# Kernel optimization log

Measured on AMD Instinct MI355X. Metric: run time of the kernel, lower is better.

Reference implementation:

```python
import jax, jax.numpy as jnp
import numpy as np

K = 16          # neighbors per point
POINTNUM = 2048 # opt.pointnum
B, N = 8, 2048


def _knn_concat(x, k):
    """x: [B,N,C] -> [B,N,k,2C] = concat(center, k-nearest neighbor feats)."""
    sq = jnp.sum(x * x, axis=-1)                                   # [B,N]
    d2 = sq[:, :, None] + sq[:, None, :] - 2.0 * jnp.einsum('bnc,bmc->bnm', x, x)
    _, idx = jax.lax.top_k(-d2, k)                                 # [B,N,k]
    nbr = jax.vmap(lambda xb, ib: xb[ib])(x, idx)                  # [B,N,k,C]
    ctr = jnp.broadcast_to(x[:, :, None, :], nbr.shape)
    return jnp.concatenate([ctr, nbr], axis=-1)


def _lin(x, w, b):
    return x @ w + b


lrelu = jax.nn.leaky_relu  # default negative_slope=0.01 matches nn.LeakyReLU()


def setup_inputs() -> dict:
    key = jax.random.key(0)
    ks = jax.random.split(key, 20)

    def w(k_, fi, fo):
        return jax.random.normal(k_, (fi, fo), jnp.float32) / np.sqrt(fi)

    inp = {
        'x': jax.random.normal(ks[0], (B, N, 3), jnp.float32),
        'h1w1': w(ks[1], 6, 16),   'h1b1': jnp.zeros((16,), jnp.float32),
        'h1w2': w(ks[2], 16, 64),  'h1b2': jnp.zeros((64,), jnp.float32),
        'h1w3': w(ks[3], 64, 32),  'h1b3': jnp.zeros((32,), jnp.float32),
        'h2w1': w(ks[4], 64, 256), 'h2b1': jnp.zeros((256,), jnp.float32),
        'h2w2': w(ks[5], 256, 128),'h2b2': jnp.zeros((128,), jnp.float32),
        'h3w1': w(ks[6], 256, 128),'h3b1': jnp.zeros((128,), jnp.float32),
        'fc1w': w(ks[7], 128, 128),'fc1b': jnp.zeros((128,), jnp.float32),
        'fc2w': w(ks[8], 128, 128),'fc2b': jnp.zeros((128,), jnp.float32),
        'fc3w': w(ks[9], 128, POINTNUM * 3), 'fc3b': jnp.zeros((POINTNUM * 3,), jnp.float32),
    }
    return inp


def reference(x, h1w1, h1b1, h1w2, h1b2, h1w3, h1b3,
              h2w1, h2b1, h2w2, h2b2, h3w1, h3b1,
              fc1w, fc1b, fc2w, fc2b, fc3w, fc3b):
    # block 1: knn-concat [B,N,K,6] -> MLP(6,16,64,32) -> sum over K
    x1 = _knn_concat(x, K)
    h = lrelu(_lin(x1, h1w1, h1b1))
    h = lrelu(_lin(h, h1w2, h1b2))
    h = lrelu(_lin(h, h1w3, h1b3))
    x2 = jnp.sum(h, axis=2)                    # [B,N,32]
    # block 2: [B,N,K,64] -> MLP(64,256,128) -> sum over K
    x2 = _knn_concat(x2, K)
    h = lrelu(_lin(x2, h2w1, h2b1))
    h = lrelu(_lin(h, h2w2, h2b2))
    x3 = jnp.sum(h, axis=2)                    # [B,N,128]
    # block 3: [B,N,K,256] -> MLP(256,128) -> sum over K
    x3 = _knn_concat(x3, K)
    h = lrelu(_lin(x3, h3w1, h3b1))
    x4 = jnp.sum(h, axis=2)                    # [B,N,128]
    # global max pool over points
    x5 = jnp.max(x4, axis=1)                   # [B,128]
    x6 = lrelu(_lin(x5, fc1w, fc1b))
    x7 = lrelu(_lin(x6, fc2w, fc2b))
    x8 = _lin(x7, fc3w, fc3b)                  # [B, POINTNUM*3]
    return x8.reshape(x8.shape[0], POINTNUM, 3)
```

## Files before the change

kernel.cpp:

```cpp
#include <hip/hip_runtime.h>

#define KNB 16
#define BSZ 8
#define NPT 2048

typedef __attribute__((ext_vector_type(8))) short bf16x8;
typedef __attribute__((ext_vector_type(4))) float f32x4;

__device__ __forceinline__ float lrelu(float x) { return x >= 0.f ? x : 0.01f * x; }

__device__ __forceinline__ unsigned short bf16rne(float f) {
    union { float f; unsigned int u; } v; v.f = f;
    return (unsigned short)((v.u + 0x7FFFu + ((v.u >> 16) & 1u)) >> 16);
}

__device__ __forceinline__ float packkey(float d, int idx) {
    union { float f; unsigned int u; } v; v.f = d;
    v.u = (v.u & 0xFFFFF800u) | (unsigned int)idx;
    return v.f;
}

__device__ __forceinline__ void ceA(float& a, float& b) {
    const float lo = fminf(a, b), hi = fmaxf(a, b);
    a = lo; b = hi;
}

__device__ __forceinline__ void bsort16(float* c) {
#pragma unroll
    for (int k = 2; k <= 16; k <<= 1) {
#pragma unroll
        for (int j = k >> 1; j > 0; j >>= 1) {
#pragma unroll
            for (int i = 0; i < 16; ++i) {
                const int l = i ^ j;
                if (l > i) {
                    if ((i & k) == 0) ceA(c[i], c[l]);
                    else              ceA(c[l], c[i]);
                }
            }
        }
    }
}

__device__ __forceinline__ void merge16(float* L, const float* C) {
#pragma unroll
    for (int i = 0; i < 16; ++i) L[i] = fminf(L[i], C[15 - i]);
#pragma unroll
    for (int j = 8; j > 0; j >>= 1) {
#pragma unroll
        for (int i = 0; i < 16; ++i) {
            const int l = i ^ j;
            if (l > i) ceA(L[i], L[l]);
        }
    }
}

__device__ __forceinline__ void st16(float* dst, const float* L) {
#pragma unroll
    for (int c = 0; c < 4; ++c)
        *(f32x4*)(dst + c * 4) = (f32x4){L[c * 4], L[c * 4 + 1], L[c * 4 + 2], L[c * 4 + 3]};
}

__device__ __forceinline__ void ld16(float* L, const float* src) {
#pragma unroll
    for (int c = 0; c < 4; ++c) {
        const f32x4 v = *(const f32x4*)(src + c * 4);
        L[c * 4] = v[0]; L[c * 4 + 1] = v[1]; L[c * 4 + 2] = v[2]; L[c * 4 + 3] = v[3];
    }
}

__device__ __forceinline__ void xwave_merge_out(float (*sS)[20], int w, int lane,
                                                float* L, float* outp) {
    st16(sS[w * 64 + lane], L);
    __syncthreads();
    if ((w & 1) == 0) {
        float C[16];
        ld16(C, sS[(w + 1) * 64 + lane]);
        merge16(L, C);
        if (w == 2) st16(sS[2 * 64 + lane], L);
    }
    __syncthreads();
    if (w == 0) {
        float C[16];
        ld16(C, sS[2 * 64 + lane]);
        merge16(L, C);
        st16(outp, L);
    }
}

__global__ void wprep_all_kernel(const float* __restrict__ h2w1, unsigned short* __restrict__ w1t,
                                 const float* __restrict__ h2w2, unsigned short* __restrict__ w2t,
                                 const float* __restrict__ h3w1, unsigned short* __restrict__ w3t,
                                 const float* __restrict__ w1, const float* __restrict__ w2,
                                 const float* __restrict__ w3,
                                 unsigned short* __restrict__ w1a, unsigned short* __restrict__ w2a,
                                 unsigned short* __restrict__ w3a) {
    const int bid = blockIdx.x, tid = threadIdx.x;
    if (bid < 64) {
        int i = bid * 256 + tid;
        int k = i >> 8, n = i & 255;
        w1t[n * 64 + k] = bf16rne(h2w1[i]);
    } else if (bid < 192) {
        int i = (bid - 64) * 256 + tid;
        int k = i >> 7, n = i & 127;
        w2t[n * 256 + k] = bf16rne(h2w2[i]);
    } else if (bid < 320) {
        int i = (bid - 192) * 256 + tid;
        int k = i >> 7, n = i & 127;
        w3t[n * 256 + k] = bf16rne(h3w1[i]);
    } else {
        int i = (bid - 320) * 256 + tid;
        if (i < 512) {
            int n = i >> 5, k = i & 31;
            w1a[i] = (k < 6) ? bf16rne(w1[k * 16 + n]) : (unsigned short)0;
        } else if (i < 2560) {
            int j = i - 512, n = j >> 5, k = j & 31;
            w2a[j] = (k < 16) ? bf16rne(w2[k * 64 + n]) : (unsigned short)0;
        } else if (i < 4608) {
            int j = i - 2560, n = j >> 6, k = j & 63;
            w3a[j] = bf16rne(w3[k * 32 + n]);
        }
    }
}

template<int C>
__global__ void norms_kernel(const float* __restrict__ feat, float* __restrict__ out) {
    int gid = blockIdx.x * blockDim.x + threadIdx.x;
    if (gid < BSZ * NPT) {
        const float* p = feat + (size_t)gid * C;
        float s = 0.f;
#pragma unroll
        for (int c = 0; c < C; ++c) s = fmaf(p[c], p[c], s);
        out[gid] = s;
    }
}

__global__ void norms16q_kernel(const unsigned short* __restrict__ feat, float* __restrict__ out) {
    const int gid = blockIdx.x * 256 + threadIdx.x;
    const int q = gid >> 2, prt = gid & 3;
    const unsigned short* p = feat + (size_t)q * 128 + prt * 32;
    float s = 0.f;
#pragma unroll
    for (int c8 = 0; c8 < 4; ++c8) {
        const bf16x8 v = *(const bf16x8*)(p + c8 * 8);
#pragma unroll
        for (int j = 0; j < 8; ++j) {
            union { unsigned int u; float f; } t;
            t.u = ((unsigned int)(unsigned short)v[j]) << 16;
            s = fmaf(t.f, t.f, s);
        }
    }
    s += __shfl_xor(s, 1);
    s += __shfl_xor(s, 2);
    if (prt == 0) out[q] = s;
}

template<int JS>
__launch_bounds__(256, 4)
__global__ void knn3_kernel(const float* __restrict__ feat,
                            const float* __restrict__ norms,
                            float* __restrict__ cand) {
    constexpr int JL = NPT / JS;
    constexpr int JP = JL / 4;
    const int idxf = blockIdx.x + 32 * (blockIdx.y + 8 * blockIdx.z);
    const int b    = idxf & 7;
    const int rem  = idxf >> 3;
    const int js   = rem & 7;
    const int i0   = (rem >> 3) * 64;
    const int t = threadIdx.x, w = t >> 6, lane = t & 63;
    const float* fb = feat + (size_t)b * NPT * 3;
    const float* nb = norms + (size_t)b * NPT;

    __shared__ __align__(16) float sS[256][20];

    float q0, q1, q2;
    { const float* qp = fb + (size_t)(i0 + lane) * 3; q0 = qp[0]; q1 = qp[1]; q2 = qp[2]; }

    float L[16];
    const int jbeg = js * JL + w * JP;
#pragma unroll 1
    for (int j0 = jbeg; j0 < jbeg + JP; j0 += 16) {
        float C[16];
#pragma unroll
        for (int u = 0; u < 16; ++u) {
            const int j = j0 + u;
            const float* pp = fb + (size_t)j * 3;
            C[u] = packkey(fmaf(-2.f, fmaf(q0, pp[0], fmaf(q1, pp[1], q2 * pp[2])), nb[j]), j);
        }
        bsort16(C);
        if (j0 == jbeg) {
#pragma unroll
            for (int u = 0; u < 16; ++u) L[u] = C[u];
        } else {
            merge16(L, C);
        }
    }
    float* o = cand + (((size_t)b * NPT + i0 + lane) * JS + js) * 16;
    xwave_merge_out(sS, w, lane, L, o);
}

template<int C, int JS>
__launch_bounds__(256, C == 32 ? 4 : 3)
__global__ void knn_mfma_kernel(const unsigned short* __restrict__ fb16,
                                const float* __restrict__ norms,
                                float* __restrict__ cand) {
    constexpr int JL = NPT / JS;
    constexpr int KS = C / 32;
    const int idxf = blockIdx.x + 32 * (blockIdx.y + 8 * blockIdx.z);
    const int b    = idxf & 7;
    const int rem  = idxf >> 3;
    const int js   = rem & 7;
    const int i0   = (rem >> 3) * 64;
    const int t    = threadIdx.x;
    const int w    = t >> 6;
    const int lane = t & 63;
    const int l15  = lane & 15;
    const int quad = lane >> 4;
    const unsigned short* fbb = fb16 + (size_t)b * NPT * C;
    const float* nb = norms + (size_t)b * NPT;

    __shared__ __align__(16) float sS[256][20];

    bf16x8 afr[KS * 4];
#pragma unroll
    for (int ks = 0; ks < KS; ++ks)
#pragma unroll
        for (int mi = 0; mi < 4; ++mi)
            afr[ks * 4 + mi] = *(const bf16x8*)(fbb + (size_t)(i0 + mi * 16 + l15) * C + ks * 32 + quad * 8);

    float L[16];
    const int jbeg = js * JL;
#pragma unroll 1
    for (int j0 = jbeg; j0 < jbeg + JL; j0 += 64) {
        f32x4 acc[4];
#pragma unroll
        for (int mi = 0; mi < 4; ++mi) acc[mi] = (f32x4){0.f, 0.f, 0.f, 0.f};
        const unsigned short* prow = fbb + (size_t)(j0 + w * 16 + l15) * C + quad * 8;
#pragma unroll
        for (int ks = 0; ks < KS; ++ks) {
            const bf16x8 bfr = *(const bf16x8*)(prow + ks * 32);
#pragma unroll
            for (int mi = 0; mi < 4; ++mi)
                acc[mi] = __builtin_amdgcn_mfma_f32_16x16x32_bf16(afr[ks * 4 + mi], bfr, acc[mi], 0, 0, 0);
        }
        const float nv  = nb[j0 + w * 16 + l15];
        const int  cidx = j0 + w * 16 + l15;
#pragma unroll
        for (int mi = 0; mi < 4; ++mi)
#pragma unroll
            for (int r = 0; r < 4; ++r)
                sS[w * 64 + mi * 16 + quad * 4 + r][l15] = packkey(fmaf(-2.f, acc[mi][r], nv), cidx);
        float Cb[16];
        ld16(Cb, sS[w * 64 + lane]);
        bsort16(Cb);
        if (j0 == jbeg) {
#pragma unroll
            for (int u = 0; u < 16; ++u) L[u] = Cb[u];
        } else {
            merge16(L, Cb);
        }
    }

    float* o = cand + (((size_t)b * NPT + i0 + lane) * JS + js) * 16;
    xwave_merge_out(sS, w, lane, L, o);
}

template<int JS>
__launch_bounds__(64)
__global__ void knn_merge_kernel(const float* __restrict__ cand, int* __restrict__ knn_out) {
    const int q = blockIdx.x * 64 + threadIdx.x;
    const float* pd = cand + (size_t)q * JS * 16;
    float L[16];
    ld16(L, pd);
#pragma unroll
    for (int s = 1; s < JS; ++s) {
        float C[16];
        ld16(C, pd + s * 16);
        merge16(L, C);
    }
    int* o = knn_out + (size_t)q * KNB;
#pragma unroll
    for (int u = 0; u < 16; ++u) {
        union { float f; unsigned int v; } z; z.f = L[u];
        o[u] = (int)(z.v & 2047u);
    }
}

__launch_bounds__(256, 3)
__global__ void block1_mfma_kernel(const float* __restrict__ x, const int* __restrict__ knn,
                                   const unsigned short* __restrict__ w1a, const float* __restrict__ b1,
                                   const unsigned short* __restrict__ w2a, const float* __restrict__ b2,
                                   const unsigned short* __restrict__ w3a, const float* __restrict__ b3,
                                   unsigned short* __restrict__ x2b, float* __restrict__ nrm) {
    const int w = threadIdx.x >> 6, lane = threadIdx.x & 63;
    const int l15 = lane & 15, quad = lane >> 4;

    const bf16x8 W1 = *(const bf16x8*)(w1a + l15 * 32 + quad * 8);
    bf16x8 W2[4];
#pragma unroll
    for (int nt = 0; nt < 4; ++nt)
        W2[nt] = *(const bf16x8*)(w2a + (nt * 16 + l15) * 32 + quad * 8);
    bf16x8 W3[2][2];
#pragma unroll
    for (int tt = 0; tt < 2; ++tt)
#pragma unroll
        for (int ks = 0; ks < 2; ++ks)
            W3[tt][ks] = *(const bf16x8*)(w3a + (tt * 16 + l15) * 64 + ks * 32 + quad * 8);
    float b1v[4], b2v[4][4], b3v[2][4];
#pragma unroll
    for (int r = 0; r < 4; ++r) b1v[r] = b1[quad * 4 + r];
#pragma unroll
    for (int nt = 0; nt < 4; ++nt)
#pragma unroll
        for (int r = 0; r < 4; ++r) b2v[nt][r] = b2[nt * 16 + quad * 4 + r];
#pragma unroll
    for (int tt = 0; tt < 2; ++tt)
#pragma unroll
        for (int r = 0; r < 4; ++r) b3v[tt][r] = b3[tt * 16 + quad * 4 + r];

    const int src0 = ((2 * quad) & 3) * 16 + l15;
    const int src1 = ((2 * quad + 1) & 3) * 16 + l15;
    const int ntsel = quad >> 1;

    const int p0 = blockIdx.x * 8 + w * 2;
#pragma unroll 2
    for (int pi = 0; pi < 2; ++pi) {
        const int p = p0 + pi, b = p >> 11, n = p & (NPT - 1);
        int d0 = 0, d1 = 0, d2 = 0;
        if (quad == 0) {
            const float* xc = x + ((size_t)b * NPT + n) * 3;
            const int jn = knn[(size_t)p * KNB + l15];
            const float* xn = x + ((size_t)b * NPT + jn) * 3;
            const unsigned s0 = bf16rne(xc[0]), s1 = bf16rne(xc[1]), s2 = bf16rne(xc[2]);
            const unsigned s3 = bf16rne(xn[0]), s4 = bf16rne(xn[1]), s5 = bf16rne(xn[2]);
            d0 = (int)(s0 | (s1 << 16));
            d1 = (int)(s2 | (s3 << 16));
            d2 = (int)(s4 | (s5 << 16));
        }
        union { int i[4]; bf16x8 v; } B1;
        B1.i[0] = d0; B1.i[1] = d1; B1.i[2] = d2; B1.i[3] = 0;
        const f32x4 a1 = __builtin_amdgcn_mfma_f32_16x16x32_bf16(W1, B1.v, (f32x4){0.f, 0.f, 0.f, 0.f}, 0, 0, 0);

        int h10, h11;
        {
            const unsigned t0 = bf16rne(lrelu(a1[0] + b1v[0]));
            const unsigned t1 = bf16rne(lrelu(a1[1] + b1v[1]));
            const unsigned t2 = bf16rne(lrelu(a1[2] + b1v[2]));
            const unsigned t3 = bf16rne(lrelu(a1[3] + b1v[3]));
            h10 = (int)(t0 | (t1 << 16));
            h11 = (int)(t2 | (t3 << 16));
        }
        union { int i[4]; bf16x8 v; } B2;
        {
            const int e0 = __shfl(h10, src0), e1 = __shfl(h11, src0);
            const int e2 = __shfl(h10, src1), e3 = __shfl(h11, src1);
            const bool val = quad < 2;
            B2.i[0] = val ? e0 : 0; B2.i[1] = val ? e1 : 0;
            B2.i[2] = val ? e2 : 0; B2.i[3] = val ? e3 : 0;
        }
        f32x4 a2[4];
#pragma unroll
        for (int nt = 0; nt < 4; ++nt)
            a2[nt] = __builtin_amdgcn_mfma_f32_16x16x32_bf16(W2[nt], B2.v, (f32x4){0.f, 0.f, 0.f, 0.f}, 0, 0, 0);
        int dpk[4][2];
#pragma unroll
        for (int nt = 0; nt < 4; ++nt) {
            const unsigned t0 = bf16rne(lrelu(a2[nt][0] + b2v[nt][0]));
            const unsigned t1 = bf16rne(lrelu(a2[nt][1] + b2v[nt][1]));
            const unsigned t2 = bf16rne(lrelu(a2[nt][2] + b2v[nt][2]));
            const unsigned t3 = bf16rne(lrelu(a2[nt][3] + b2v[nt][3]));
            dpk[nt][0] = (int)(t0 | (t1 << 16));
            dpk[nt][1] = (int)(t2 | (t3 << 16));
        }
        f32x4 a3[2] = { (f32x4){0.f, 0.f, 0.f, 0.f}, (f32x4){0.f, 0.f, 0.f, 0.f} };
#pragma unroll
        for (int ks = 0; ks < 2; ++ks) {
            union { int i[4]; bf16x8 v; } B3;
            const int a0l = __shfl(dpk[2 * ks][0], src0), a0h = __shfl(dpk[2 * ks + 1][0], src0);
            const int a1l = __shfl(dpk[2 * ks][1], src0), a1h = __shfl(dpk[2 * ks + 1][1], src0);
            const int a2l = __shfl(dpk[2 * ks][0], src1), a2h = __shfl(dpk[2 * ks + 1][0], src1);
            const int a3l = __shfl(dpk[2 * ks][1], src1), a3h = __shfl(dpk[2 * ks + 1][1], src1);
            B3.i[0] = ntsel ? a0h : a0l;
            B3.i[1] = ntsel ? a1h : a1l;
            B3.i[2] = ntsel ? a2h : a2l;
            B3.i[3] = ntsel ? a3h : a3l;
#pragma unroll
            for (int tt = 0; tt < 2; ++tt)
                a3[tt] = __builtin_amdgcn_mfma_f32_16x16x32_bf16(W3[tt][ks], B3.v, a3[tt], 0, 0, 0);
        }
        float na = 0.f;
#pragma unroll
        for (int tt = 0; tt < 2; ++tt) {
#pragma unroll
            for (int r = 0; r < 4; ++r) {
                float s = lrelu(a3[tt][r] + b3v[tt][r]);
                s += __shfl_xor(s, 1);
                s += __shfl_xor(s, 2);
                s += __shfl_xor(s, 4);
                s += __shfl_xor(s, 8);
                na = fmaf(s, s, na);
                if (l15 == 0)
                    x2b[(size_t)p * 32 + tt * 16 + quad * 4 + r] = bf16rne(s);
            }
        }
        na += __shfl_xor(na, 16);
        na += __shfl_xor(na, 32);
        if (lane == 0) nrm[p] = na;
    }
}

__launch_bounds__(512, 4)
__global__ void block2_fused_kernel(const unsigned short* __restrict__ x2b,
                                    const int* __restrict__ knn,
                                    const unsigned short* __restrict__ w1t,
                                    const float* __restrict__ b1,
                                    const unsigned short* __restrict__ w2t,
                                    const float* __restrict__ b2,
                                    unsigned short* __restrict__ x3b) {
    const int w    = threadIdx.x >> 6;
    const int lane = threadIdx.x & 63;
    const int l15  = lane & 15, quad = lane >> 4;
    __shared__ __align__(16) unsigned short sH1[2][16][264];
    __shared__ __align__(16) unsigned short sA2[16][17][40];

    bf16x8 B1[2][2];
#pragma unroll
    for (int nt2 = 0; nt2 < 2; ++nt2)
#pragma unroll
        for (int ks = 0; ks < 2; ++ks)
            B1[nt2][ks] = *(const bf16x8*)(w1t + (size_t)(w * 32 + nt2 * 16 + l15) * 64 + ks * 32 + quad * 8);
    bf16x8 B2[8];
#pragma unroll
    for (int ks = 0; ks < 8; ++ks)
        B2[ks] = *(const bf16x8*)(w2t + (size_t)(w * 16 + l15) * 256 + ks * 32 + quad * 8);
    float b1v[2];
#pragma unroll
    for (int nt2 = 0; nt2 < 2; ++nt2) b1v[nt2] = b1[w * 32 + nt2 * 16 + l15];
    const float b2v = b2[w * 16 + l15];

    const int src = (blockIdx.x & 7) * 128 + (blockIdx.x >> 3);
    const int p0 = src * 16;
    const unsigned short* xb = x2b + (size_t)(p0 >> 11) * NPT * 32;

    {
        const int pA = p0 + 2 * w, pB = pA + 1;
        const int nA = knn[(size_t)pA * KNB + l15];
        const int nB = knn[(size_t)pB * KNB + l15];
        *(bf16x8*)&sA2[2 * w][l15][quad * 8] =
            *(const bf16x8*)(xb + (size_t)nA * 32 + quad * 8);
        *(bf16x8*)&sA2[2 * w + 1][l15][quad * 8] =
            *(const bf16x8*)(xb + (size_t)nB * 32 + quad * 8);
        if (l15 == 0) {
            *(bf16x8*)&sA2[2 * w][16][quad * 8] =
                *(const bf16x8*)(x2b + (size_t)pA * 32 + quad * 8);
            *(bf16x8*)&sA2[2 * w + 1][16][quad * 8] =
                *(const bf16x8*)(x2b + (size_t)pB * 32 + quad * 8);
        }
    }
    __syncthreads();

#pragma unroll 1
    for (int pi = 0; pi < 16; ++pi) {
        const int p = p0 + pi, buf = pi & 1;
        const bf16x8 a0 = *(const bf16x8*)&sA2[pi][16][quad * 8];
        const bf16x8 a1 = *(const bf16x8*)&sA2[pi][l15][quad * 8];
#pragma unroll
        for (int nt2 = 0; nt2 < 2; ++nt2) {
            f32x4 acc = (f32x4){0.f, 0.f, 0.f, 0.f};
            acc = __builtin_amdgcn_mfma_f32_16x16x32_bf16(a0, B1[nt2][0], acc, 0, 0, 0);
            acc = __builtin_amdgcn_mfma_f32_16x16x32_bf16(a1, B1[nt2][1], acc, 0, 0, 0);
#pragma unroll
            for (int r = 0; r < 4; ++r)
                sH1[buf][quad * 4 + r][w * 32 + nt2 * 16 + l15] = bf16rne(lrelu(acc[r] + b1v[nt2]));
        }
        __syncthreads();
        bf16x8 afA[4], afB[4];
#pragma unroll
        for (int ks = 0; ks < 4; ++ks)
            afA[ks] = *(const bf16x8*)&sH1[buf][l15][ks * 32 + quad * 8];
#pragma unroll
        for (int ks = 0; ks < 4; ++ks)
            afB[ks] = *(const bf16x8*)&sH1[buf][l15][128 + ks * 32 + quad * 8];
        f32x4 accA = (f32x4){0.f, 0.f, 0.f, 0.f}, accB = (f32x4){0.f, 0.f, 0.f, 0.f};
#pragma unroll
        for (int ks = 0; ks < 4; ++ks) {
            accA = __builtin_amdgcn_mfma_f32_16x16x32_bf16(afA[ks], B2[ks], accA, 0, 0, 0);
            accB = __builtin_amdgcn_mfma_f32_16x16x32_bf16(afB[ks], B2[4 + ks], accB, 0, 0, 0);
        }
        float s = 0.f;
#pragma unroll
        for (int r = 0; r < 4; ++r) s += lrelu(accA[r] + accB[r] + b2v);
        s += __shfl_xor(s, 16);
        s += __shfl_xor(s, 32);
        if (quad == 0) x3b[(size_t)p * 128 + w * 16 + l15] = bf16rne(s);
    }
}

__launch_bounds__(512, 4)
__global__ void block3_fused_kernel(const unsigned short* __restrict__ x3b,
                                    const int* __restrict__ knn,
                                    const unsigned short* __restrict__ w3t,
                                    const float* __restrict__ bias,
                                    float* __restrict__ x4) {
    const int w    = threadIdx.x >> 6;
    const int lane = threadIdx.x & 63;
    const int l15  = lane & 15, quad = lane >> 4;
    __shared__ __align__(16) unsigned short sA[8][17][132];

    bf16x8 B3[8];
#pragma unroll
    for (int ks = 0; ks < 8; ++ks)
        B3[ks] = *(const bf16x8*)(w3t + (size_t)(w * 16 + l15) * 256 + ks * 32 + quad * 8);
    const float bv = bias[w * 16 + l15];

    const int src = (blockIdx.x & 7) * 256 + (blockIdx.x >> 3);
    const int p0 = src * 8;
    const unsigned short* xb = x3b + (size_t)(p0 >> 11) * NPT * 128;

    {
        const int p = p0 + w;
        const int nbr = knn[(size_t)p * KNB + l15];
        const unsigned short* nrow = xb + (size_t)nbr * 128;
#pragma unroll
        for (int c = 0; c < 4; ++c) {
            const bf16x8 v = *(const bf16x8*)(nrow + (c * 4 + quad) * 8);
            *(bf16x8*)&sA[w][l15][(c * 4 + quad) * 8] = v;
        }
        if (quad == 0) {
            const bf16x8 v = *(const bf16x8*)(x3b + (size_t)p * 128 + l15 * 8);
            *(bf16x8*)&sA[w][16][l15 * 8] = v;
        }
    }
    __syncthreads();

#pragma unroll 2
    for (int pi = 0; pi < 8; ++pi) {
        bf16x8 afA[4], afB[4];
#pragma unroll
        for (int ks = 0; ks < 4; ++ks) {
            afA[ks] = *(const bf16x8*)&sA[pi][16][(ks * 4 + quad) * 8];
            afB[ks] = *(const bf16x8*)&sA[pi][l15][(ks * 4 + quad) * 8];
        }
        f32x4 accA = (f32x4){0.f, 0.f, 0.f, 0.f}, accB = (f32x4){0.f, 0.f, 0.f, 0.f};
#pragma unroll
        for (int ks = 0; ks < 4; ++ks) {
            accA = __builtin_amdgcn_mfma_f32_16x16x32_bf16(afA[ks], B3[ks], accA, 0, 0, 0);
            accB = __builtin_amdgcn_mfma_f32_16x16x32_bf16(afB[ks], B3[4 + ks], accB, 0, 0, 0);
        }
        float s = 0.f;
#pragma unroll
        for (int r = 0; r < 4; ++r) s += lrelu(accA[r] + accB[r] + bv);
        s += __shfl_xor(s, 16);
        s += __shfl_xor(s, 32);
        if (quad == 0) x4[(size_t)(p0 + pi) * 128 + w * 16 + l15] = s;
    }
}

__launch_bounds__(128)
__global__ void maxpool_partial_kernel(const float* __restrict__ x4,
                                       float* __restrict__ part) {
    const int chunk = blockIdx.x, b = blockIdx.y, t = threadIdx.x;
    const float* xb = x4 + ((size_t)b * NPT + (size_t)chunk * 64) * 128;
    float m = -1e30f;
#pragma unroll 8
    for (int n = 0; n < 64; ++n) m = fmaxf(m, xb[(size_t)n * 128 + t]);
    part[((size_t)b * 32 + chunk) * 128 + t] = m;
}

__launch_bounds__(128)
__global__ void head2_kernel(const float* __restrict__ part,
                             const float* __restrict__ fc1w, const float* __restrict__ fc1b,
                             const float* __restrict__ fc2w, const float* __restrict__ fc2b,
                             const float* __restrict__ fc3w, const float* __restrict__ fc3b,
                             float* __restrict__ out) {
    const int g = blockIdx.x, b = blockIdx.y, t = threadIdx.x;
    __shared__ float s5[128], s6[128], s7[128];
    float m = -1e30f;
#pragma unroll
    for (int c = 0; c < 32; ++c)
        m = fmaxf(m, part[((size_t)b * 32 + c) * 128 + t]);
    s5[t] = m;
    __syncthreads();
    float a = fc1b[t];
#pragma unroll 4
    for (int i = 0; i < 128; ++i) a = fmaf(s5[i], fc1w[i * 128 + t], a);
    s6[t] = lrelu(a);
    __syncthreads();
    a = fc2b[t];
#pragma unroll 4
    for (int i = 0; i < 128; ++i) a = fmaf(s6[i], fc2w[i * 128 + t], a);
    s7[t] = lrelu(a);
    __syncthreads();
    const int o = g * 128 + t;
    float acc = fc3b[o];
#pragma unroll 4
    for (int i = 0; i < 128; ++i) acc = fmaf(s7[i], fc3w[(size_t)i * 6144 + o], acc);
    out[(size_t)b * 6144 + o] = acc;
}

extern "C" void kernel_launch(void* const* d_in, const int* in_sizes, int n_in,
                              void* d_out, int out_size, void* d_ws, size_t ws_size,
                              hipStream_t stream) {
    const float* x    = (const float*)d_in[0];
    const float* h1w1 = (const float*)d_in[1];
    const float* h1b1 = (const float*)d_in[2];
    const float* h1w2 = (const float*)d_in[3];
    const float* h1b2 = (const float*)d_in[4];
    const float* h1w3 = (const float*)d_in[5];
    const float* h1b3 = (const float*)d_in[6];
    const float* h2w1 = (const float*)d_in[7];
    const float* h2b1 = (const float*)d_in[8];
    const float* h2w2 = (const float*)d_in[9];
    const float* h2b2 = (const float*)d_in[10];
    const float* h3w1 = (const float*)d_in[11];
    const float* h3b1 = (const float*)d_in[12];
    const float* fc1w = (const float*)d_in[13];
    const float* fc1b = (const float*)d_in[14];
    const float* fc2w = (const float*)d_in[15];
    const float* fc2b = (const float*)d_in[16];
    const float* fc3w = (const float*)d_in[17];
    const float* fc3b = (const float*)d_in[18];

    float* ws = (float*)d_ws;
    unsigned short* x2b16 = (unsigned short*)ws;
    unsigned short* x3b16 = (unsigned short*)(ws + 262144);
    float* x4   = ws + 1310720;
    float* cd   = x4;
    int*   idx  = (int*)(ws + 3407872);
    float* nrm  = ws + 3670016;
    unsigned short* w1t = (unsigned short*)(ws + 3702784);
    unsigned short* w2t = (unsigned short*)(ws + 3710976);
    unsigned short* w3t = (unsigned short*)(ws + 3727360);
    unsigned short* w1a = (unsigned short*)(ws + 3743744);
    unsigned short* w2a = (unsigned short*)(ws + 3744000);
    unsigned short* w3a = (unsigned short*)(ws + 3745024);
    float* part = ws + 3746048;
    float* out  = (float*)d_out;

    const dim3 kg(32, 8, 8);

    wprep_all_kernel<<<338, 256, 0, stream>>>(h2w1, w1t, h2w2, w2t, h3w1, w3t,
                                              h1w1, h1w2, h1w3, w1a, w2a, w3a);

    norms_kernel<3><<<64, 256, 0, stream>>>(x, nrm);
    knn3_kernel<8><<<kg, 256, 0, stream>>>(x, nrm, cd);
    knn_merge_kernel<8><<<256, 64, 0, stream>>>(cd, idx);
    block1_mfma_kernel<<<2048, 256, 0, stream>>>(x, idx, w1a, h1b1, w2a, h1b2, w3a, h1b3,
                                                 x2b16, nrm);

    knn_mfma_kernel<32, 8><<<kg, 256, 0, stream>>>(x2b16, nrm, cd);
    knn_merge_kernel<8><<<256, 64, 0, stream>>>(cd, idx);
    block2_fused_kernel<<<BSZ * NPT / 16, 512, 0, stream>>>(x2b16, idx, w1t, h2b1, w2t, h2b2, x3b16);

    norms16q_kernel<<<256, 256, 0, stream>>>(x3b16, nrm);
    knn_mfma_kernel<128, 8><<<kg, 256, 0, stream>>>(x3b16, nrm, cd);
    knn_merge_kernel<8><<<256, 64, 0, stream>>>(cd, idx);
    block3_fused_kernel<<<BSZ * NPT / 8, 512, 0, stream>>>(x3b16, idx, w3t, h3b1, x4);

    maxpool_partial_kernel<<<dim3(32, 8), 128, 0, stream>>>(x4, part);
    head2_kernel<<<dim3(48, 8), 128, 0, stream>>>(part, fc1w, fc1b, fc2w, fc2b,
                                                  fc3w, fc3b, out);
}
```

Baseline: 340.2 us.

## Fuse block3 norm computation into block2, use packed bf16 converts, stage A fragments

Removes the standalone norms16q kernel by computing the squared norms of the rounded bf16 block-2 outputs inside block2_fused_kernel through shuffle reductions and a small shared buffer. Replaces the manual bf16 rounding and packing with the hardware v_cvt_pk_bf16_f32 instruction and rewrites leaky ReLU as a fmax. Loads the 128-channel A fragments in the kNN kernel through shared memory with coalesced row loads. This saves a launch and a pass over x3, but adds a block-wide sync and extra LDS use to the kNN kernel.

```diff
diff --git a/kernel.cpp b/kernel.cpp
--- a/kernel.cpp
+++ b/kernel.cpp
@@ -7,11 +7,17 @@
 typedef __attribute__((ext_vector_type(8))) short bf16x8;
 typedef __attribute__((ext_vector_type(4))) float f32x4;
 
-__device__ __forceinline__ float lrelu(float x) { return x >= 0.f ? x : 0.01f * x; }
+__device__ __forceinline__ float lrelu(float x) { return fmaxf(x, 0.01f * x); }
 
 __device__ __forceinline__ unsigned short bf16rne(float f) {
     union { float f; unsigned int u; } v; v.f = f;
     return (unsigned short)((v.u + 0x7FFFu + ((v.u >> 16) & 1u)) >> 16);
+}
+
+__device__ __forceinline__ unsigned int cvt_pk_bf16(float lo, float hi) {
+    unsigned int r;
+    asm("v_cvt_pk_bf16_f32 %0, %1, %2" : "=v"(r) : "v"(lo), "v"(hi));
+    return r;
 }
 
 __device__ __forceinline__ float packkey(float d, int idx) {
@@ -135,26 +141,6 @@
     }
 }
 
-__global__ void norms16q_kernel(const unsigned short* __restrict__ feat, float* __restrict__ out) {
-    const int gid = blockIdx.x * 256 + threadIdx.x;
-    const int q = gid >> 2, prt = gid & 3;
-    const unsigned short* p = feat + (size_t)q * 128 + prt * 32;
-    float s = 0.f;
-#pragma unroll
-    for (int c8 = 0; c8 < 4; ++c8) {
-        const bf16x8 v = *(const bf16x8*)(p + c8 * 8);
-#pragma unroll
-        for (int j = 0; j < 8; ++j) {
-            union { unsigned int u; float f; } t;
-            t.u = ((unsigned int)(unsigned short)v[j]) << 16;
-            s = fmaf(t.f, t.f, s);
-        }
-    }
-    s += __shfl_xor(s, 1);
-    s += __shfl_xor(s, 2);
-    if (prt == 0) out[q] = s;
-}
-
 template<int JS>
 __launch_bounds__(256, 4)
 __global__ void knn3_kernel(const float* __restrict__ feat,
@@ -222,11 +208,30 @@
     __shared__ __align__(16) float sS[256][20];
 
     bf16x8 afr[KS * 4];
-#pragma unroll
-    for (int ks = 0; ks < KS; ++ks)
-#pragma unroll
-        for (int mi = 0; mi < 4; ++mi)
-            afr[ks * 4 + mi] = *(const bf16x8*)(fbb + (size_t)(i0 + mi * 16 + l15) * C + ks * 32 + quad * 8);
+    if constexpr (C == 128) {
+        __shared__ __align__(16) unsigned short sAF[64][132];
+        {
+            const int row = t >> 2, c4 = t & 3;
+#pragma unroll
+            for (int c = 0; c < 4; ++c) {
+                const int chunk = c4 * 4 + c;
+                *(bf16x8*)&sAF[row][chunk * 8] =
+                    *(const bf16x8*)(fbb + (size_t)(i0 + row) * 128 + chunk * 8);
+            }
+        }
+        __syncthreads();
+#pragma unroll
+        for (int ks = 0; ks < KS; ++ks)
+#pragma unroll
+            for (int mi = 0; mi < 4; ++mi)
+                afr[ks * 4 + mi] = *(const bf16x8*)&sAF[mi * 16 + l15][ks * 32 + quad * 8];
+    } else {
+#pragma unroll
+        for (int ks = 0; ks < KS; ++ks)
+#pragma unroll
+            for (int mi = 0; mi < 4; ++mi)
+                afr[ks * 4 + mi] = *(const bf16x8*)(fbb + (size_t)(i0 + mi * 16 + l15) * C + ks * 32 + quad * 8);
+    }
 
     float L[16];
     const int jbeg = js * JL;
@@ -341,15 +346,8 @@
         B1.i[0] = d0; B1.i[1] = d1; B1.i[2] = d2; B1.i[3] = 0;
         const f32x4 a1 = __builtin_amdgcn_mfma_f32_16x16x32_bf16(W1, B1.v, (f32x4){0.f, 0.f, 0.f, 0.f}, 0, 0, 0);
 
-        int h10, h11;
-        {
-            const unsigned t0 = bf16rne(lrelu(a1[0] + b1v[0]));
-            const unsigned t1 = bf16rne(lrelu(a1[1] + b1v[1]));
-            const unsigned t2 = bf16rne(lrelu(a1[2] + b1v[2]));
-            const unsigned t3 = bf16rne(lrelu(a1[3] + b1v[3]));
-            h10 = (int)(t0 | (t1 << 16));
-            h11 = (int)(t2 | (t3 << 16));
-        }
+        const int h10 = (int)cvt_pk_bf16(lrelu(a1[0] + b1v[0]), lrelu(a1[1] + b1v[1]));
+        const int h11 = (int)cvt_pk_bf16(lrelu(a1[2] + b1v[2]), lrelu(a1[3] + b1v[3]));
         union { int i[4]; bf16x8 v; } B2;
         {
             const int e0 = __shfl(h10, src0), e1 = __shfl(h11, src0);
@@ -365,12 +363,8 @@
         int dpk[4][2];
 #pragma unroll
         for (int nt = 0; nt < 4; ++nt) {
-            const unsigned t0 = bf16rne(lrelu(a2[nt][0] + b2v[nt][0]));
-            const unsigned t1 = bf16rne(lrelu(a2[nt][1] + b2v[nt][1]));
-            const unsigned t2 = bf16rne(lrelu(a2[nt][2] + b2v[nt][2]));
-            const unsigned t3 = bf16rne(lrelu(a2[nt][3] + b2v[nt][3]));
-            dpk[nt][0] = (int)(t0 | (t1 << 16));
-            dpk[nt][1] = (int)(t2 | (t3 << 16));
+            dpk[nt][0] = (int)cvt_pk_bf16(lrelu(a2[nt][0] + b2v[nt][0]), lrelu(a2[nt][1] + b2v[nt][1]));
+            dpk[nt][1] = (int)cvt_pk_bf16(lrelu(a2[nt][2] + b2v[nt][2]), lrelu(a2[nt][3] + b2v[nt][3]));
         }
         f32x4 a3[2] = { (f32x4){0.f, 0.f, 0.f, 0.f}, (f32x4){0.f, 0.f, 0.f, 0.f} };
 #pragma unroll
@@ -416,12 +410,14 @@
                                     const float* __restrict__ b1,
                                     const unsigned short* __restrict__ w2t,
                                     const float* __restrict__ b2,
-                                    unsigned short* __restrict__ x3b) {
+                                    unsigned short* __restrict__ x3b,
+                                    float* __restrict__ nrm2) {
     const int w    = threadIdx.x >> 6;
     const int lane = threadIdx.x & 63;
     const int l15  = lane & 15, quad = lane >> 4;
     __shared__ __align__(16) unsigned short sH1[2][16][264];
     __shared__ __align__(16) unsigned short sA2[16][17][40];
+    __shared__ float sNrm[16][8];
 
     bf16x8 B1[2][2];
 #pragma unroll
@@ -469,9 +465,13 @@
             f32x4 acc = (f32x4){0.f, 0.f, 0.f, 0.f};
             acc = __builtin_amdgcn_mfma_f32_16x16x32_bf16(a0, B1[nt2][0], acc, 0, 0, 0);
             acc = __builtin_amdgcn_mfma_f32_16x16x32_bf16(a1, B1[nt2][1], acc, 0, 0, 0);
-#pragma unroll
-            for (int r = 0; r < 4; ++r)
-                sH1[buf][quad * 4 + r][w * 32 + nt2 * 16 + l15] = bf16rne(lrelu(acc[r] + b1v[nt2]));
+            const unsigned int u01 = cvt_pk_bf16(lrelu(acc[0] + b1v[nt2]), lrelu(acc[1] + b1v[nt2]));
+            const unsigned int u23 = cvt_pk_bf16(lrelu(acc[2] + b1v[nt2]), lrelu(acc[3] + b1v[nt2]));
+            const int ch = w * 32 + nt2 * 16 + l15;
+            sH1[buf][quad * 4 + 0][ch] = (unsigned short)u01;
+            sH1[buf][quad * 4 + 1][ch] = (unsigned short)(u01 >> 16);
+            sH1[buf][quad * 4 + 2][ch] = (unsigned short)u23;
+            sH1[buf][quad * 4 + 3][ch] = (unsigned short)(u23 >> 16);
         }
         __syncthreads();
         bf16x8 afA[4], afB[4];
@@ -492,7 +492,25 @@
         for (int r = 0; r < 4; ++r) s += lrelu(accA[r] + accB[r] + b2v);
         s += __shfl_xor(s, 16);
         s += __shfl_xor(s, 32);
-        if (quad == 0) x3b[(size_t)p * 128 + w * 16 + l15] = bf16rne(s);
+        const unsigned short us = bf16rne(s);
+        if (quad == 0) x3b[(size_t)p * 128 + w * 16 + l15] = us;
+        union { unsigned int u; float f; } sb; sb.u = ((unsigned int)us) << 16;
+        float na = sb.f * sb.f;
+        na += __shfl_xor(na, 1);
+        na += __shfl_xor(na, 2);
+        na += __shfl_xor(na, 4);
+        na += __shfl_xor(na, 8);
+        if (lane == 0) sNrm[pi][w] = na;
+    }
+
+    __syncthreads();
+    if (threadIdx.x < 128) {
+        const int pi = threadIdx.x >> 3, wv = threadIdx.x & 7;
+        float v = sNrm[pi][wv];
+        v += __shfl_xor(v, 1);
+        v += __shfl_xor(v, 2);
+        v += __shfl_xor(v, 4);
+        if (wv == 0) nrm2[p0 + pi] = v;
     }
 }
 
@@ -650,9 +668,9 @@
 
     knn_mfma_kernel<32, 8><<<kg, 256, 0, stream>>>(x2b16, nrm, cd);
     knn_merge_kernel<8><<<256, 64, 0, stream>>>(cd, idx);
-    block2_fused_kernel<<<BSZ * NPT / 16, 512, 0, stream>>>(x2b16, idx, w1t, h2b1, w2t, h2b2, x3b16);
-
-    norms16q_kernel<<<256, 256, 0, stream>>>(x3b16, nrm);
+    block2_fused_kernel<<<BSZ * NPT / 16, 512, 0, stream>>>(x2b16, idx, w1t, h2b1, w2t, h2b2,
+                                                            x3b16, nrm);
+
     knn_mfma_kernel<128, 8><<<kg, 256, 0, stream>>>(x3b16, nrm, cd);
     knn_merge_kernel<8><<<256, 64, 0, stream>>>(cd, idx);
     block3_fused_kernel<<<BSZ * NPT / 8, 512, 0, stream>>>(x3b16, idx, w3t, h3b1, x4);
```

Result: faster. 326.6 us (-4.0%).
